# Optimization experiments

Hardware: AMD Instinct MI355X
Metric: run time of the kernel (lower is better)

Reference implementation:

```python
import jax, jax.numpy as jnp
import numpy as np

HEADS = 16
HEAD_DIM = 128
HIDDEN = HEADS * HEAD_DIM  # 2048
B = 4
S = 2048  # max (padded) sequence length


def setup_inputs() -> dict:
    key = jax.random.key(0)
    k1, k2, k3 = jax.random.split(key, 3)
    x = jax.random.normal(k1, (B, S, HIDDEN), dtype=jnp.float32)
    W_qkv = jax.random.normal(k2, (HIDDEN, 3 * HIDDEN), dtype=jnp.float32) * 0.02
    b_qkv = jax.random.normal(k3, (3 * HIDDEN,), dtype=jnp.float32) * 0.02
    # jagged lengths mirroring the source's TOKENS // (i + 1) pattern
    lengths = jnp.array([S // (i + 1) for i in range(B)], dtype=jnp.int64)
    return {"x": x, "W_qkv": W_qkv, "b_qkv": b_qkv, "lengths": lengths}


def reference(x, W_qkv, b_qkv, lengths):
    # x: [B, S, HIDDEN] padded jagged batch; lengths: [B] valid token counts
    qkv = x @ W_qkv + b_qkv                       # [B, S, 3*HIDDEN]
    q, k, v = jnp.split(qkv, 3, axis=-1)          # each [B, S, HIDDEN]

    def to_heads(t):  # [B, S, HIDDEN] -> [B, H, S, D]
        return t.reshape(B, S, HEADS, HEAD_DIM).transpose(0, 2, 1, 3)

    q, k, v = to_heads(q), to_heads(k), to_heads(v)

    scale = 1.0 / jnp.sqrt(jnp.asarray(HEAD_DIM, dtype=q.dtype))
    scores = jnp.einsum('bhqd,bhkd->bhqk', q, k) * scale  # [B, H, S, S]

    valid = jnp.arange(S)[None, :] < lengths[:, None]     # [B, S]
    neg = jnp.asarray(-1e30, dtype=scores.dtype)
    scores = jnp.where(valid[:, None, None, :], scores, neg)

    attn = jax.nn.softmax(scores, axis=-1)                # [B, H, S, S]
    out = jnp.einsum('bhqk,bhkd->bhqd', attn, v)          # [B, H, S, D]
    # zero out padded query rows (they don't exist in the nested tensor)
    out = out * valid[:, None, :, None].astype(out.dtype)
    return out
```

## Files before the change

### kernel.cpp

```cpp
#include <hip/hip_runtime.h>
#include <stdint.h>

#define BATCH 4
#define SEQ   2048
#define NH    16
#define HD    128
#define HID   2048
#define N3    6144

typedef _Float16 f16;
typedef _Float16 f16x8 __attribute__((ext_vector_type(8)));
typedef _Float16 f16x4 __attribute__((ext_vector_type(4)));
typedef float    f32x4 __attribute__((ext_vector_type(4)));

#define QSCALE 0.1275313895f

__device__ __forceinline__ int get_len(const int* L, int b) {
  return (L[1] == 0) ? L[2 * b] : L[b];
}

__device__ __forceinline__ void async_copy16(void* lds_uniform, const void* gptr) {
  __builtin_amdgcn_global_load_lds(
      (const __attribute__((address_space(1))) void*)(uintptr_t)gptr,
      (__attribute__((address_space(3))) void*)(uint32_t)(uintptr_t)lds_uniform,
      16, 0, 0);
}

__global__ __launch_bounds__(256) void cvt_fused(const float* __restrict__ x,
                                                 f16* __restrict__ xh,
                                                 const float* __restrict__ W,
                                                 f16* __restrict__ Wt) {
  __shared__ float tile[64][65];
  if (blockIdx.x < 8192) {
    int idx = blockIdx.x * 256 + threadIdx.x;
    int m = idx >> 8;
    int g = idx & 255;
    int p = (g & ~3) | ((g ^ ((m >> 1) & 3)) & 3);
    const float* src = x + (size_t)m * HID + g * 8;
    f16x8 o;
#pragma unroll
    for (int j = 0; j < 8; ++j) o[j] = (f16)src[j];
    *(f16x8*)&xh[(size_t)m * HID + p * 8] = o;
  } else {
    int bid = blockIdx.x - 8192;
    const int n0 = (bid % 96) * 64;
    const int k0 = (bid / 96) * 64;
    const int tid = threadIdx.x;
#pragma unroll
    for (int i = 0; i < 4; ++i) {
      int id = tid + i * 256;
      int kr = id >> 4, nc = id & 15;
      f32x4 v = *(const f32x4*)&W[(size_t)(k0 + kr) * N3 + n0 + nc * 4];
#pragma unroll
      for (int j = 0; j < 4; ++j) tile[kr][nc * 4 + j] = v[j];
    }
    __syncthreads();
#pragma unroll
    for (int i = 0; i < 2; ++i) {
      int id = tid + i * 256;
      int nl = id >> 3;
      int kc = id & 7;
      f16x8 o;
#pragma unroll
      for (int j = 0; j < 8; ++j) o[j] = (f16)tile[kc * 8 + j][nl];
      int n = n0 + nl;
      int gk = (k0 >> 3) + kc;
      int p = (gk & ~3) | ((gk ^ ((n >> 1) & 3)) & 3);
      *(f16x8*)&Wt[(size_t)n * HID + p * 8] = o;
    }
  }
}

__global__ __launch_bounds__(256, 3)
void qkv_gemm(const f16* __restrict__ xh, const f16* __restrict__ Wt,
              const float* __restrict__ bias, const int* __restrict__ lens,
              f16* __restrict__ Qh, f16* __restrict__ Kh, f16* __restrict__ Vt) {
  __shared__ f16 As[2 * 128 * 32];
  __shared__ f16 Bs[2 * 128 * 32];

  const int tid = threadIdx.x;
  const int wave = tid >> 6, lane = tid & 63;
  const int lr = lane & 15, quad = lane >> 4;
  const int nblk = blockIdx.x;
  const int mblk = blockIdx.y;
  const int m0 = mblk * 128;
  const int b = m0 >> 11;
  const int s0 = m0 & (SEQ - 1);
  const int len = get_len(lens, b);
  if (s0 >= len) return;
  const int n0 = nblk * 128;
  const int wr = (wave >> 1) * 64;
  const int wc = (wave & 1) * 64;

  f32x4 acc[4][4] = {};
  const char* xbase = (const char*)xh + (size_t)m0 * (HID * 2);
  const char* wbase = (const char*)Wt + (size_t)n0 * (HID * 2);

  for (int k0 = 0; k0 < HID; k0 += 64) {
    __syncthreads();
#pragma unroll
    for (int i = 0; i < 4; ++i) {
      int slot = wave * 4 + i;
      int hh = slot >> 3;
      int sub = slot & 7;
      int row = sub * 16 + (lane >> 2);
      size_t gcol = (size_t)k0 * 2 + hh * 64 + (lane & 3) * 16;
      async_copy16(&As[slot * 512], xbase + (size_t)row * (HID * 2) + gcol);
      async_copy16(&Bs[slot * 512], wbase + (size_t)row * (HID * 2) + gcol);
    }
    __syncthreads();

#pragma unroll
    for (int hh = 0; hh < 2; ++hh) {
      f16x8 a[4], bf[4];
#pragma unroll
      for (int mt = 0; mt < 4; ++mt) {
        int row = wr + mt * 16 + lr;
        int c = quad ^ ((row >> 1) & 3);
        a[mt] = *(const f16x8*)&As[hh * 4096 + row * 32 + c * 8];
      }
#pragma unroll
      for (int nt = 0; nt < 4; ++nt) {
        int row = wc + nt * 16 + lr;
        int c = quad ^ ((row >> 1) & 3);
        bf[nt] = *(const f16x8*)&Bs[hh * 4096 + row * 32 + c * 8];
      }
#pragma unroll
      for (int mt = 0; mt < 4; ++mt)
#pragma unroll
        for (int nt = 0; nt < 4; ++nt)
          acc[mt][nt] = __builtin_amdgcn_mfma_f32_16x16x32_f16(a[mt], bf[nt],
                                                               acc[mt][nt], 0, 0, 0);
    }
  }

  const int t = nblk >> 4;
  const int h = nblk & 15;
  const size_t bhoff = (size_t)(b * NH + h);

  if (t == 0) {
    f16* qp = Qh + bhoff * (SEQ * HD);
#pragma unroll
    for (int nt = 0; nt < 4; ++nt) {
      int d = wc + nt * 16 + lr;
      float bv = bias[n0 + d];
#pragma unroll
      for (int mt = 0; mt < 4; ++mt) {
        int sb = s0 + wr + mt * 16 + quad * 4;
#pragma unroll
        for (int r = 0; r < 4; ++r)
          qp[(size_t)(sb + r) * HD + d] = (f16)((acc[mt][nt][r] + bv) * QSCALE);
      }
    }
  } else if (t == 1) {
    f16* kp = Kh + bhoff * (SEQ * HD);
#pragma unroll
    for (int nt = 0; nt < 4; ++nt) {
      int d = wc + nt * 16 + lr;
      float bv = bias[n0 + d];
#pragma unroll
      for (int mt = 0; mt < 4; ++mt) {
        int sb = s0 + wr + mt * 16 + quad * 4;
#pragma unroll
        for (int r = 0; r < 4; ++r) {
          int s = sb + r;
          int c = (d >> 3) ^ (s & 15);
          kp[(size_t)s * HD + c * 8 + (d & 7)] = (f16)(acc[mt][nt][r] + bv);
        }
      }
    }
  } else {
    f16* vp = Vt + bhoff * (HD * SEQ);
#pragma unroll
    for (int nt = 0; nt < 4; ++nt) {
      int d = wc + nt * 16 + lr;
      float bv = bias[n0 + d];
#pragma unroll
      for (int mt = 0; mt < 4; ++mt) {
        int sb = s0 + wr + mt * 16 + quad * 4;
        f16x4 pk;
#pragma unroll
        for (int r = 0; r < 4; ++r) pk[r] = (f16)(acc[mt][nt][r] + bv);
        int p = (sb >> 3) ^ (d & 7);
        *(f16x4*)&vp[(size_t)d * SEQ + p * 8 + (sb & 7)] = pk;
      }
    }
  }
}

__global__ __launch_bounds__(256, 3)
void attn(const f16* __restrict__ Qh, const f16* __restrict__ Kh,
          const f16* __restrict__ Vt, const int* __restrict__ lens,
          float* __restrict__ out) {
  __shared__ f16 Ks[64 * 128];
  __shared__ f16 Vs[128 * 64];

  const int tid = threadIdx.x, wave = tid >> 6, lane = tid & 63;
  const int lr = lane & 15, quad = lane >> 4;
  const int id = blockIdx.x;
  const int bhlo = id & 7;
  const int r3 = id >> 3;
  const int qt = r3 & 15;
  const int bh = ((r3 >> 4) << 3) | bhlo;
  const int b = bh >> 4, h = bh & 15;
  const int len = get_len(lens, b);
  const int q0 = qt * 128;
  const size_t bho = (size_t)(b * NH + h);
  float* obase = out + bho * (size_t)(SEQ * HD);

  if (q0 >= len) {
    f32x4 z = {0.f, 0.f, 0.f, 0.f};
#pragma unroll
    for (int i = 0; i < 16; ++i) {
      int idx = tid + i * 256;
      *(f32x4*)&obase[(size_t)q0 * HD + (size_t)idx * 4] = z;
    }
    return;
  }

  f16x8 qa[2][4];
  {
    const f16* qp = Qh + bho * (size_t)(SEQ * HD);
#pragma unroll
    for (int rg = 0; rg < 2; ++rg) {
      int row = q0 + wave * 32 + rg * 16 + lr;
#pragma unroll
      for (int ks = 0; ks < 4; ++ks)
        qa[rg][ks] = *(const f16x8*)&qp[(size_t)row * HD + ks * 32 + quad * 8];
    }
  }

  float lrow[2] = {0.f, 0.f};
  f32x4 oacc[2][8] = {};

  const char* kpl = (const char*)(Kh + bho * (size_t)(SEQ * HD));
  const char* vpl = (const char*)(Vt + bho * (size_t)(HD * SEQ));

  const int nkt = (len + 63) >> 6;

  auto stageK = [&](int kt) {
    size_t koff = (size_t)kt * 64;
#pragma unroll
    for (int j = 0; j < 4; ++j) {
      int slot = wave * 4 + j;
      const char* src = kpl +
          ((koff + slot * 4 + (lane >> 4)) * HD + (size_t)(lane & 15) * 8) * 2;
      async_copy16(&Ks[slot * 512], src);
    }
  };
  auto stageV = [&](int kt) {
    size_t koff = (size_t)kt * 64;
#pragma unroll
    for (int j = 0; j < 4; ++j) {
      int slot = wave * 4 + j;
      const char* src = vpl +
          ((size_t)(slot * 8 + (lane >> 3)) * SEQ + koff + (size_t)(lane & 7) * 8) * 2;
      async_copy16(&Vs[slot * 512], src);
    }
  };

  stageK(0);
  stageV(0);
  asm volatile("s_waitcnt vmcnt(0)" ::: "memory");
  __builtin_amdgcn_s_barrier();

  for (int kt = 0; kt < nkt; ++kt) {
    f32x4 sacc[2][4] = {};
#pragma unroll
    for (int ks = 0; ks < 4; ++ks) {
      f16x8 kb[4];
#pragma unroll
      for (int nt = 0; nt < 4; ++nt) {
        int key = nt * 16 + lr;
        int c = (ks * 4 + quad) ^ (key & 15);
        kb[nt] = *(const f16x8*)&Ks[key * 128 + c * 8];
      }
#pragma unroll
      for (int nt = 0; nt < 4; ++nt) {
        sacc[0][nt] = __builtin_amdgcn_mfma_f32_16x16x32_f16(kb[nt], qa[0][ks],
                                                             sacc[0][nt], 0, 0, 0);
        sacc[1][nt] = __builtin_amdgcn_mfma_f32_16x16x32_f16(kb[nt], qa[1][ks],
                                                             sacc[1][nt], 0, 0, 0);
      }
    }

    const int kbase = kt * 64;
    if (kbase + 64 > len) {
#pragma unroll
      for (int nt = 0; nt < 4; ++nt)
#pragma unroll
        for (int r = 0; r < 4; ++r)
          if (kbase + nt * 16 + quad * 4 + r >= len) {
            sacc[0][nt][r] = -3.0e38f;
            sacc[1][nt][r] = -3.0e38f;
          }
    }

    f16x4 pb[2][4];
#pragma unroll
    for (int rg = 0; rg < 2; ++rg)
#pragma unroll
      for (int nt = 0; nt < 4; ++nt) {
        float e0 = __builtin_amdgcn_exp2f(sacc[rg][nt][0]);
        float e1 = __builtin_amdgcn_exp2f(sacc[rg][nt][1]);
        float e2 = __builtin_amdgcn_exp2f(sacc[rg][nt][2]);
        float e3 = __builtin_amdgcn_exp2f(sacc[rg][nt][3]);
        lrow[rg] += (e0 + e1) + (e2 + e3);
        f16x4 pk = {(f16)e0, (f16)e1, (f16)e2, (f16)e3};
        pb[rg][nt] = pk;
      }

    const int ktn = (kt + 1 < nkt) ? kt + 1 : nkt - 1;
    asm volatile("s_waitcnt vmcnt(0)" ::: "memory");
    __builtin_amdgcn_s_barrier();
    stageK(ktn);

#pragma unroll
    for (int dt = 0; dt < 8; ++dt) {
      int d = dt * 16 + lr;
      f16x4 va[4];
#pragma unroll
      for (int nt = 0; nt < 4; ++nt) {
        int cc = (nt * 2 + (quad >> 1)) ^ (d & 7);
        va[nt] = *(const f16x4*)&Vs[d * 64 + cc * 8 + (quad & 1) * 4];
      }
#pragma unroll
      for (int nt = 0; nt < 4; ++nt) {
        oacc[0][dt] = __builtin_amdgcn_mfma_f32_16x16x16f16(va[nt], pb[0][nt],
                                                            oacc[0][dt], 0, 0, 0);
        oacc[1][dt] = __builtin_amdgcn_mfma_f32_16x16x16f16(va[nt], pb[1][nt],
                                                            oacc[1][dt], 0, 0, 0);
      }
    }

    __builtin_amdgcn_s_barrier();
    stageV(ktn);
    asm volatile("s_waitcnt vmcnt(4)" ::: "memory");
    __builtin_amdgcn_s_barrier();
  }
  asm volatile("s_waitcnt vmcnt(0)" ::: "memory");

  float linv[2];
#pragma unroll
  for (int rg = 0; rg < 2; ++rg) {
    float l = lrow[rg];
    l += __shfl_xor(l, 16);
    l += __shfl_xor(l, 32);
    linv[rg] = 1.0f / l;
  }
#pragma unroll
  for (int rg = 0; rg < 2; ++rg) {
    int s = q0 + wave * 32 + rg * 16 + lr;
    bool valid = s < len;
#pragma unroll
    for (int dt = 0; dt < 8; ++dt) {
      f32x4 o;
#pragma unroll
      for (int r = 0; r < 4; ++r)
        o[r] = valid ? oacc[rg][dt][r] * linv[rg] : 0.0f;
      *(f32x4*)&obase[(size_t)s * HD + dt * 16 + quad * 4] = o;
    }
  }
}

extern "C" void kernel_launch(void* const* d_in, const int* in_sizes, int n_in,
                              void* d_out, int out_size, void* d_ws, size_t ws_size,
                              hipStream_t stream) {
  const float* x = (const float*)d_in[0];
  const float* W = (const float*)d_in[1];
  const float* bias = (const float*)d_in[2];
  const int* lens = (const int*)d_in[3];
  float* out = (float*)d_out;

  char* ws = (char*)d_ws;
  size_t off = 0;
  f16* xh = (f16*)(ws + off); off += (size_t)BATCH * SEQ * HID * 2;
  f16* Wt = (f16*)(ws + off); off += (size_t)N3 * HID * 2;
  f16* Qh = (f16*)(ws + off); off += (size_t)BATCH * NH * SEQ * HD * 2;
  f16* Kh = (f16*)(ws + off); off += (size_t)BATCH * NH * SEQ * HD * 2;
  f16* Vt = (f16*)(ws + off); off += (size_t)BATCH * NH * SEQ * HD * 2;

  cvt_fused<<<8192 + 3072, 256, 0, stream>>>(x, xh, W, Wt);
  qkv_gemm<<<dim3(48, 64), 256, 0, stream>>>(xh, Wt, bias, lens, Qh, Kh, Vt);
  attn<<<1024, 256, 0, stream>>>(Qh, Kh, Vt, lens, out);
}
```

Baseline: 372.7 us.

## Double-buffer K and V tiles in attention to overlap loads with compute

```diff
diff --git a/kernel.cpp b/kernel.cpp
--- a/kernel.cpp
+++ b/kernel.cpp
@@ -188,12 +188,12 @@
   }
 }
 
-__global__ __launch_bounds__(256, 3)
+__global__ __launch_bounds__(256, 2)
 void attn(const f16* __restrict__ Qh, const f16* __restrict__ Kh,
           const f16* __restrict__ Vt, const int* __restrict__ lens,
           float* __restrict__ out) {
-  __shared__ f16 Ks[64 * 128];
-  __shared__ f16 Vs[128 * 64];
+  __shared__ f16 Ks[2][64 * 128];
+  __shared__ f16 Vs[2][128 * 64];
 
   const int tid = threadIdx.x, wave = tid >> 6, lane = tid & 63;
   const int lr = lane & 15, quad = lane >> 4;
@@ -238,33 +238,39 @@
 
   const int nkt = (len + 63) >> 6;
 
-  auto stageK = [&](int kt) {
+  auto stageK = [&](int bf, int kt) {
     size_t koff = (size_t)kt * 64;
 #pragma unroll
     for (int j = 0; j < 4; ++j) {
       int slot = wave * 4 + j;
       const char* src = kpl +
           ((koff + slot * 4 + (lane >> 4)) * HD + (size_t)(lane & 15) * 8) * 2;
-      async_copy16(&Ks[slot * 512], src);
+      async_copy16(&Ks[bf][slot * 512], src);
     }
   };
-  auto stageV = [&](int kt) {
+  auto stageV = [&](int bf, int kt) {
     size_t koff = (size_t)kt * 64;
 #pragma unroll
     for (int j = 0; j < 4; ++j) {
       int slot = wave * 4 + j;
       const char* src = vpl +
           ((size_t)(slot * 8 + (lane >> 3)) * SEQ + koff + (size_t)(lane & 7) * 8) * 2;
-      async_copy16(&Vs[slot * 512], src);
+      async_copy16(&Vs[bf][slot * 512], src);
     }
   };
 
-  stageK(0);
-  stageV(0);
+  stageK(0, 0);
+  stageV(0, 0);
   asm volatile("s_waitcnt vmcnt(0)" ::: "memory");
   __builtin_amdgcn_s_barrier();
 
   for (int kt = 0; kt < nkt; ++kt) {
+    const int cur = kt & 1;
+    if (kt + 1 < nkt) {
+      stageK(cur ^ 1, kt + 1);
+      stageV(cur ^ 1, kt + 1);
+    }
+
     f32x4 sacc[2][4] = {};
 #pragma unroll
     for (int ks = 0; ks < 4; ++ks) {
@@ -273,7 +279,7 @@
       for (int nt = 0; nt < 4; ++nt) {
         int key = nt * 16 + lr;
         int c = (ks * 4 + quad) ^ (key & 15);
-        kb[nt] = *(const f16x8*)&Ks[key * 128 + c * 8];
+        kb[nt] = *(const f16x8*)&Ks[cur][key * 128 + c * 8];
       }
 #pragma unroll
       for (int nt = 0; nt < 4; ++nt) {
@@ -310,11 +316,6 @@
         pb[rg][nt] = pk;
       }
 
-    const int ktn = (kt + 1 < nkt) ? kt + 1 : nkt - 1;
-    asm volatile("s_waitcnt vmcnt(0)" ::: "memory");
-    __builtin_amdgcn_s_barrier();
-    stageK(ktn);
-
 #pragma unroll
     for (int dt = 0; dt < 8; ++dt) {
       int d = dt * 16 + lr;
@@ -322,7 +323,7 @@
 #pragma unroll
       for (int nt = 0; nt < 4; ++nt) {
         int cc = (nt * 2 + (quad >> 1)) ^ (d & 7);
-        va[nt] = *(const f16x4*)&Vs[d * 64 + cc * 8 + (quad & 1) * 4];
+        va[nt] = *(const f16x4*)&Vs[cur][d * 64 + cc * 8 + (quad & 1) * 4];
       }
 #pragma unroll
       for (int nt = 0; nt < 4; ++nt) {
@@ -333,12 +334,9 @@
       }
     }
 
+    asm volatile("s_waitcnt vmcnt(0)" ::: "memory");
     __builtin_amdgcn_s_barrier();
-    stageV(ktn);
-    asm volatile("s_waitcnt vmcnt(4)" ::: "memory");
-    __builtin_amdgcn_s_barrier();
-  }
-  asm volatile("s_waitcnt vmcnt(0)" ::: "memory");
+  }
 
   float linv[2];
 #pragma unroll
```

After: 333.7 us. 10.5% less time.
